# Kernel tuning notes

Measured on AMD Instinct MI355X. Metric: run time of the kernel, lower is better.

## Reference

```python
import jax, jax.numpy as jnp
import numpy as np

N, D = 4096, 784

def _conv_relu(x, w, b):
    y = jax.lax.conv_general_dilated(x, w, window_strides=(1, 1), padding='SAME',
                                     dimension_numbers=('NHWC', 'HWIO', 'NHWC'))
    return jax.nn.relu(y + b)

def _maxpool2(x):
    return jax.lax.reduce_window(x, -jnp.inf, jax.lax.max,
                                 (1, 2, 2, 1), (1, 2, 2, 1), 'SAME')

def _encoder(x, cw1, cb1, cw2, cb2, cw3, cb3, dw, db):
    h = x.reshape(-1, 28, 28, 1)
    h = _maxpool2(_conv_relu(h, cw1, cb1))   # [N,14,14,32]
    h = _maxpool2(_conv_relu(h, cw2, cb2))   # [N,7,7,32]
    h = _conv_relu(h, cw3, cb3)              # [N,7,7,16]
    h = h.reshape(h.shape[0], -1)            # [N,784]
    return h @ dw + db                       # [N,16]

def _pairwise_dist(a):
    # Euclidean cdist via Gram trick; avoids the O(N^2 * D) broadcasted diff.
    sq = jnp.sum(a * a, axis=-1)
    d2 = sq[:, None] + sq[None, :] - 2.0 * (a @ a.T)
    return jnp.sqrt(jnp.maximum(d2, 1e-12))

def setup_inputs() -> dict:
    key = jax.random.key(0)
    ks = jax.random.split(key, 5)
    return {
        'x':   jax.random.uniform(ks[0], (N, D), dtype=jnp.float32),
        'cw1': jax.random.normal(ks[1], (3, 3, 1, 32), dtype=jnp.float32) * 0.1,
        'cb1': jnp.zeros((32,), jnp.float32),
        'cw2': jax.random.normal(ks[2], (3, 3, 32, 32), dtype=jnp.float32) * 0.05,
        'cb2': jnp.zeros((32,), jnp.float32),
        'cw3': jax.random.normal(ks[3], (3, 3, 32, 16), dtype=jnp.float32) * 0.05,
        'cb3': jnp.zeros((16,), jnp.float32),
        'dw':  jax.random.normal(ks[4], (D, 16), dtype=jnp.float32) * 0.05,
        'db':  jnp.zeros((16,), jnp.float32),
        'nnfactor': 64,
    }

def reference(x, cw1, cb1, cw2, cb2, cw3, cb3, dw, db, nnfactor):
    n = x.shape[0]
    k = n // nnfactor  # as in train_step
    encoded = _encoder(x, cw1, cb1, cw2, cb2, cw3, cb3, dw, db)
    # tensor_get_nearest (faithful: tf.nn.top_k takes LARGEST distances)
    d_ini = _pairwise_dist(x)                       # [N,N]
    vals_ini, idx = jax.lax.top_k(d_ini, k - 1)     # sorted descending
    vals_ini = vals_ini[:, 1:]                      # [N,k-2]
    idx = idx[:, 1:]
    d_enc = _pairwise_dist(encoded)                 # [N,N]
    vals_enc = jnp.take_along_axis(d_enc, idx, axis=1)
    multiple = jnp.mean(vals_ini / vals_enc)
    reduced = vals_enc * multiple
    # per-row custom loss: max squared error, then mean over batch
    losses = jnp.max(jnp.square(vals_ini - reduced), axis=1)  # [N]
    total_loss = jnp.sum(losses) / n
    return total_loss
```

## Files before the change

kernel.cpp:

```cpp
#include <hip/hip_runtime.h>
#include <math.h>

#define NN 4096
#define DIM 784
#define K62 62
#define CAP 128

__global__ __launch_bounds__(256) void k_sqnorm(const float* __restrict__ x, double* __restrict__ sqnd,
                                                float* __restrict__ sqnf) {
    int r = blockIdx.x * 4 + (threadIdx.x >> 6);
    int lane = threadIdx.x & 63;
    const float* xr = x + (size_t)r * DIM;
    double s = 0.0;
    for (int k = lane; k < DIM; k += 64) { double v = (double)xr[k]; s += v * v; }
    for (int o = 32; o > 0; o >>= 1) s += __shfl_down(s, o);
    if (lane == 0) { sqnd[r] = s; sqnf[r] = (float)s; }
}

#define F4C(v, i) ((i) == 0 ? (v).x : (i) == 1 ? (v).y : (i) == 2 ? (v).z : (v).w)

__device__ __forceinline__ unsigned pk16(float a, float b) {
    return (__float_as_uint(a) >> 16) | (__float_as_uint(b) & 0xFFFF0000u);
}

__global__ __launch_bounds__(256, 4) void k_encgram(const float* __restrict__ x,
    const float* __restrict__ cw1, const float* __restrict__ cb1,
    const float* __restrict__ cw2, const float* __restrict__ cb2,
    const float* __restrict__ cw3, const float* __restrict__ cb3,
    const float* __restrict__ dw, const float* __restrict__ db,
    const float* __restrict__ sqnf,
    unsigned short* __restrict__ Dm16, double* __restrict__ Enc, double* __restrict__ esqd)
{
    __shared__ __align__(16) unsigned char SB[17408];
    int t = threadIdx.x;

    if (blockIdx.x < 1056) {
        float* As = (float*)SB;
        float* Bs = (float*)(SB + 8192);
        unsigned short* Cs16 = (unsigned short*)SB;
        int id = blockIdx.x >> 1, pass = blockIdx.x & 1;
        int bi = (int)((sqrtf(8.f * (float)id + 1.f) - 1.f) * 0.5f);
        while ((bi + 1) * (bi + 2) / 2 <= id) ++bi;
        while (bi * (bi + 1) / 2 > id) --bi;
        int bj = id - bi * (bi + 1) / 2;
        int i0 = bi * 128, j0 = bj * 128;
        int tx = t & 15, ty = t >> 4;
        int lrow = t >> 1, lk = (t & 1) * 8;
        int wl = lrow + ((lrow >> 5) << 2);
        int bofs = tx * 8 + ((tx >> 2) << 2);
        const float* arow = x + (size_t)(i0 + lrow) * DIM + lk;
        const float* brow = x + (size_t)(j0 + lrow) * DIM + lk;

        float acc[4][8];
        #pragma unroll
        for (int r = 0; r < 4; ++r)
        #pragma unroll
        for (int c = 0; c < 8; ++c) acc[r][c] = 0.f;
        int abase = ty * 8 + pass * 4;
        for (int kk = 0; kk < DIM; kk += 16) {
            float4 a0 = *(const float4*)(arow + kk);
            float4 a1 = *(const float4*)(arow + kk + 4);
            float4 b0 = *(const float4*)(brow + kk);
            float4 b1 = *(const float4*)(brow + kk + 4);
            __syncthreads();
            As[(lk + 0) * 128 + lrow] = a0.x; As[(lk + 1) * 128 + lrow] = a0.y;
            As[(lk + 2) * 128 + lrow] = a0.z; As[(lk + 3) * 128 + lrow] = a0.w;
            As[(lk + 4) * 128 + lrow] = a1.x; As[(lk + 5) * 128 + lrow] = a1.y;
            As[(lk + 6) * 128 + lrow] = a1.z; As[(lk + 7) * 128 + lrow] = a1.w;
            Bs[(lk + 0) * 140 + wl] = b0.x; Bs[(lk + 1) * 140 + wl] = b0.y;
            Bs[(lk + 2) * 140 + wl] = b0.z; Bs[(lk + 3) * 140 + wl] = b0.w;
            Bs[(lk + 4) * 140 + wl] = b1.x; Bs[(lk + 5) * 140 + wl] = b1.y;
            Bs[(lk + 6) * 140 + wl] = b1.z; Bs[(lk + 7) * 140 + wl] = b1.w;
            __syncthreads();
            #pragma unroll
            for (int k = 0; k < 16; ++k) {
                float4 av  = *(const float4*)&As[k * 128 + abase];
                const float* bp = &Bs[k * 140 + bofs];
                float4 bv0 = *(const float4*)bp;
                float4 bv1 = *(const float4*)(bp + 4);
                float a[4]  = {av.x, av.y, av.z, av.w};
                float bb[8] = {bv0.x, bv0.y, bv0.z, bv0.w, bv1.x, bv1.y, bv1.z, bv1.w};
                #pragma unroll
                for (int r = 0; r < 4; ++r)
                #pragma unroll
                for (int c = 0; c < 8; ++c) acc[r][c] = fmaf(a[r], bb[c], acc[r][c]);
            }
        }
        float si[4], sj[8];
        #pragma unroll
        for (int r = 0; r < 4; ++r) si[r] = sqnf[i0 + abase + r];
        #pragma unroll
        for (int c = 0; c < 8; ++c) sj[c] = sqnf[j0 + tx * 8 + c];
        #pragma unroll
        for (int r = 0; r < 4; ++r) {
            #pragma unroll
            for (int c = 0; c < 8; ++c) acc[r][c] = fmaxf(si[r] + sj[c] - 2.f * acc[r][c], 1e-12f);
            uint4 u;
            u.x = pk16(acc[r][0], acc[r][1]);
            u.y = pk16(acc[r][2], acc[r][3]);
            u.z = pk16(acc[r][4], acc[r][5]);
            u.w = pk16(acc[r][6], acc[r][7]);
            *(uint4*)(Dm16 + (size_t)(i0 + abase + r) * NN + j0 + tx * 8) = u;
        }
        if (bi != bj) {
            for (int qr = 0; qr < 2; ++qr)
            for (int qc = 0; qc < 2; ++qc) {
                __syncthreads();
                {
                    int a32 = t >> 3, c8 = t & 7;
                    int l = ((a32 >> 2) << 3) + pass * 4 + (a32 & 3);
                    uint4 v = *(const uint4*)&Dm16[(size_t)(i0 + qr * 64 + l) * NN + j0 + qc * 64 + c8 * 8];
                    int cb = c8 * 8;
                    Cs16[(cb + 0) * 36 + a32] = (unsigned short)(v.x);
                    Cs16[(cb + 1) * 36 + a32] = (unsigned short)(v.x >> 16);
                    Cs16[(cb + 2) * 36 + a32] = (unsigned short)(v.y);
                    Cs16[(cb + 3) * 36 + a32] = (unsigned short)(v.y >> 16);
                    Cs16[(cb + 4) * 36 + a32] = (unsigned short)(v.z);
                    Cs16[(cb + 5) * 36 + a32] = (unsigned short)(v.z >> 16);
                    Cs16[(cb + 6) * 36 + a32] = (unsigned short)(v.w);
                    Cs16[(cb + 7) * 36 + a32] = (unsigned short)(v.w >> 16);
                }
                __syncthreads();
                #pragma unroll
                for (int g = 0; g < 2; ++g) {
                    int idx = t + g * 256;
                    int a = idx >> 3, grp = idx & 7;
                    uint2 v = *(const uint2*)&Cs16[a * 36 + grp * 4];
                    *(uint2*)&Dm16[(size_t)(j0 + qc * 64 + a) * NN + i0 + qr * 64 + grp * 8 + pass * 4] = v;
                }
            }
        }
        return;
    }

    float*  sb1  = (float*)(SB);
    float*  sb2  = (float*)(SB + 128);
    float*  sb3  = (float*)(SB + 256);
    float*  sdb  = (float*)(SB + 320);
    float*  scw1 = (float*)(SB + 384);
    float*  wq   = (float*)(SB + 1536);
    float*  simg = (float*)(SB + 6144);
    float*  h1q  = (float*)(SB + 9744);
    float*  wq3  = (float*)(SB + 1536);
    float*  h2s  = (float*)(SB + 6144);
    float*  c3   = (float*)(SB + 6144);
    double* red  = (double*)(SB + 14768);
    double* se   = (double*)(SB + 16816);

    int n = blockIdx.x - 1056;
    for (int idx = t; idx < 1280; idx += 256) h1q[idx] = 0.f;
    for (int idx = t; idx < 900; idx += 256) simg[idx] = 0.f;
    __syncthreads();
    if (t < 196) {
        int row = t / 7, c4 = t % 7;
        float4 v = ((const float4*)(x + (size_t)n * DIM))[t];
        float* d = &simg[(row + 1) * 30 + 1 + c4 * 4];
        d[0] = v.x; d[1] = v.y; d[2] = v.z; d[3] = v.w;
    }
    for (int idx = t; idx < 288; idx += 256) scw1[idx] = cw1[idx];
    if (t < 32) { sb1[t] = cb1[t]; sb2[t] = cb2[t]; }
    if (t < 16) { sb3[t] = cb3[t]; sdb[t] = db[t]; }
    __syncthreads();

    int p2 = t >> 2, co8 = (t & 3) * 8;
    int py2 = p2 / 7, px2 = p2 % 7;
    int cbase = ((2 * py2) * 16 + 2 * px2) * 5;
    int ch1 = t & 3;
    float acc[4][8];
    if (t < 196) {
        #pragma unroll
        for (int pp = 0; pp < 4; ++pp)
        #pragma unroll
        for (int q = 0; q < 8; ++q) acc[pp][q] = sb2[co8 + q];
    }

    for (int oct = 0; oct < 8; ++oct) {
        __syncthreads();
        {
            int co = (oct << 2) + ch1;
            float wv[9];
            #pragma unroll
            for (int tp = 0; tp < 9; ++tp) wv[tp] = scw1[tp * 32 + co];
            float bias = sb1[co];
            for (int o = t; o < 784; o += 256) {
                int p = o >> 2;
                int py = p / 14, px = p % 14;
                float m = 0.f;
                #pragma unroll
                for (int dy = 0; dy < 2; ++dy)
                #pragma unroll
                for (int dx = 0; dx < 2; ++dx) {
                    const float* sp = &simg[(2 * py + dy + 1) * 30 + (2 * px + dx + 1)];
                    float a = bias;
                    a = fmaf(sp[-31], wv[0], a);
                    a = fmaf(sp[-30], wv[1], a);
                    a = fmaf(sp[-29], wv[2], a);
                    a = fmaf(sp[ -1], wv[3], a);
                    a = fmaf(sp[  0], wv[4], a);
                    a = fmaf(sp[  1], wv[5], a);
                    a = fmaf(sp[ 29], wv[6], a);
                    a = fmaf(sp[ 30], wv[7], a);
                    a = fmaf(sp[ 31], wv[8], a);
                    if (a < 0.f) a = 0.f;
                    if (a > m) m = a;
                }
                h1q[((py + 1) * 16 + (px + 1)) * 5 + ch1] = m;
            }
        }
        for (int w2 = t; w2 < 1152; w2 += 256) {
            int tap = w2 >> 7, k = w2 & 127;
            wq[w2] = cw2[tap * 1024 + oct * 128 + k];
        }
        __syncthreads();
        if (t < 196) {
            #pragma unroll
            for (int ky = 0; ky < 3; ++ky)
            #pragma unroll
            for (int kx = 0; kx < 3; ++kx) {
                const float* wb0 = &wq[(ky * 3 + kx) * 128 + co8];
                const float* hb = &h1q[cbase + (ky * 16 + kx) * 5];
                #pragma unroll
                for (int ci = 0; ci < 4; ++ci) {
                    float4 wA = *(const float4*)(wb0 + ci * 32);
                    float4 wB = *(const float4*)(wb0 + ci * 32 + 4);
                    float v00 = hb[ci];
                    float v01 = hb[5 + ci];
                    float v10 = hb[80 + ci];
                    float v11 = hb[85 + ci];
                    acc[0][0] = fmaf(v00, wA.x, acc[0][0]); acc[0][1] = fmaf(v00, wA.y, acc[0][1]);
                    acc[0][2] = fmaf(v00, wA.z, acc[0][2]); acc[0][3] = fmaf(v00, wA.w, acc[0][3]);
                    acc[0][4] = fmaf(v00, wB.x, acc[0][4]); acc[0][5] = fmaf(v00, wB.y, acc[0][5]);
                    acc[0][6] = fmaf(v00, wB.z, acc[0][6]); acc[0][7] = fmaf(v00, wB.w, acc[0][7]);
                    acc[1][0] = fmaf(v01, wA.x, acc[1][0]); acc[1][1] = fmaf(v01, wA.y, acc[1][1]);
                    acc[1][2] = fmaf(v01, wA.z, acc[1][2]); acc[1][3] = fmaf(v01, wA.w, acc[1][3]);
                    acc[1][4] = fmaf(v01, wB.x, acc[1][4]); acc[1][5] = fmaf(v01, wB.y, acc[1][5]);
                    acc[1][6] = fmaf(v01, wB.z, acc[1][6]); acc[1][7] = fmaf(v01, wB.w, acc[1][7]);
                    acc[2][0] = fmaf(v10, wA.x, acc[2][0]); acc[2][1] = fmaf(v10, wA.y, acc[2][1]);
                    acc[2][2] = fmaf(v10, wA.z, acc[2][2]); acc[2][3] = fmaf(v10, wA.w, acc[2][3]);
                    acc[2][4] = fmaf(v10, wB.x, acc[2][4]); acc[2][5] = fmaf(v10, wB.y, acc[2][5]);
                    acc[2][6] = fmaf(v10, wB.z, acc[2][6]); acc[2][7] = fmaf(v10, wB.w, acc[2][7]);
                    acc[3][0] = fmaf(v11, wA.x, acc[3][0]); acc[3][1] = fmaf(v11, wA.y, acc[3][1]);
                    acc[3][2] = fmaf(v11, wA.z, acc[3][2]); acc[3][3] = fmaf(v11, wA.w, acc[3][3]);
                    acc[3][4] = fmaf(v11, wB.x, acc[3][4]); acc[3][5] = fmaf(v11, wB.y, acc[3][5]);
                    acc[3][6] = fmaf(v11, wB.z, acc[3][6]); acc[3][7] = fmaf(v11, wB.w, acc[3][7]);
                }
            }
        }
    }
    __syncthreads();
    if (t < 196) {
        float mm[8];
        #pragma unroll
        for (int q = 0; q < 8; ++q) {
            float m = 0.f;
            #pragma unroll
            for (int pp = 0; pp < 4; ++pp) {
                float a = acc[pp][q];
                if (a < 0.f) a = 0.f;
                if (a > m) m = a;
            }
            mm[q] = m;
        }
        *(float4*)&h2s[p2 * 44 + co8]     = make_float4(mm[0], mm[1], mm[2], mm[3]);
        *(float4*)&h2s[p2 * 44 + co8 + 4] = make_float4(mm[4], mm[5], mm[6], mm[7]);
    }
    float a0 = 0.f, a1 = 0.f, a2 = 0.f, a3 = 0.f;
    int p3 = t >> 2, co4 = (t & 3) * 4;
    int py3 = p3 / 7, px3 = p3 % 7;
    if (t < 196) {
        a0 = sb3[co4]; a1 = sb3[co4 + 1];
        a2 = sb3[co4 + 2]; a3 = sb3[co4 + 3];
    }
    for (int qq = 0; qq < 4; ++qq) {
        __syncthreads();
        for (int w2 = t; w2 < 1152; w2 += 256) {
            int tap = w2 >> 7, k = w2 & 127;
            wq3[w2] = cw3[tap * 512 + qq * 128 + k];
        }
        __syncthreads();
        if (t < 196) {
            for (int ky = 0; ky < 3; ++ky) {
                int iy = py3 + ky - 1; if ((unsigned)iy >= 7u) continue;
                for (int kx = 0; kx < 3; ++kx) {
                    int ix = px3 + kx - 1; if ((unsigned)ix >= 7u) continue;
                    const float* hp = &h2s[(iy * 7 + ix) * 44 + qq * 8];
                    float4 h0 = *(const float4*)hp;
                    float4 h1 = *(const float4*)(hp + 4);
                    const float* wp = &wq3[(ky * 3 + kx) * 128 + co4];
                    #pragma unroll
                    for (int ci = 0; ci < 8; ++ci) {
                        float av = (ci < 4) ? F4C(h0, ci) : F4C(h1, ci - 4);
                        float4 wv = *(const float4*)(wp + ci * 16);
                        a0 = fmaf(av, wv.x, a0); a1 = fmaf(av, wv.y, a1);
                        a2 = fmaf(av, wv.z, a2); a3 = fmaf(av, wv.w, a3);
                    }
                }
            }
        }
    }
    __syncthreads();
    if (t < 196) {
        float r0 = a0 > 0.f ? a0 : 0.f, r1 = a1 > 0.f ? a1 : 0.f;
        float r2 = a2 > 0.f ? a2 : 0.f, r3 = a3 > 0.f ? a3 : 0.f;
        *(float4*)&c3[p3 * 16 + co4] = make_float4(r0, r1, r2, r3);
    }
    __syncthreads();
    {
        int part = t >> 4, o = t & 15, j0 = part * 49;
        double s = 0.0;
        for (int j = 0; j < 49; ++j) s = fma((double)c3[j0 + j], (double)dw[(size_t)(j0 + j) * 16 + o], s);
        red[part * 16 + o] = s;
    }
    __syncthreads();
    if (t < 16) {
        double e = (double)sdb[t];
        for (int q = 0; q < 16; ++q) e += red[q * 16 + t];
        Enc[(size_t)n * 16 + t] = e;
        se[t] = e;
    }
    __syncthreads();
    if (t == 0) {
        double s = 0.0;
        for (int q = 0; q < 16; ++q) s += se[q] * se[q];
        esqd[n] = s;
    }
}

__global__ __launch_bounds__(256) void k_topsel(const unsigned short* __restrict__ Dm16,
                                                const double* __restrict__ sqnd,
                                                const float* __restrict__ x,
                                                double* __restrict__ topvd, int* __restrict__ topi) {
    __shared__ float xi[DIM];
    __shared__ unsigned wsum[8];
    __shared__ int cj[CAP];
    __shared__ double cvd[CAP];
    __shared__ unsigned ncnt;
    int i = blockIdx.x, t = threadIdx.x;
    const unsigned* drow = (const unsigned*)(Dm16 + (size_t)i * NN);
    unsigned uk[8];
    #pragma unroll
    for (int s = 0; s < 8; ++s) {
        int wd = t + s * 256;
        unsigned u = drow[wd];
        if (2 * wd == i)     u &= 0xFFFF0000u;
        if (2 * wd + 1 == i) u &= 0x0000FFFFu;
        uk[s] = u;
    }
    if (t < 196) ((float4*)xi)[t] = ((const float4*)(x + (size_t)i * DIM))[t];
    if (t == 0) ncnt = 0;
    int lane = t & 63, w = t >> 6;
    unsigned lo = 0u, hi = 0xFFFFu;
    for (int it = 0; it < 16; ++it) {
        unsigned mid = (lo + hi + 1u) >> 1;
        unsigned cnt = 0;
        #pragma unroll
        for (int s = 0; s < 8; ++s) {
            cnt += ((uk[s] & 0xFFFFu) >= mid) ? 1u : 0u;
            cnt += ((uk[s] >> 16) >= mid) ? 1u : 0u;
        }
        #pragma unroll
        for (int off = 32; off > 0; off >>= 1) cnt += __shfl_down(cnt, off);
        if (lane == 0) wsum[(it & 1) * 4 + w] = cnt;
        __syncthreads();
        int bb = (it & 1) * 4;
        unsigned tot = wsum[bb] + wsum[bb + 1] + wsum[bb + 2] + wsum[bb + 3];
        if (tot >= 63u) lo = mid; else hi = mid - 1u;
    }
    unsigned prefix = lo;
    #pragma unroll
    for (int s = 0; s < 8; ++s) {
        int wd = t + s * 256;
        if ((uk[s] & 0xFFFFu) >= prefix) {
            unsigned p = atomicAdd(&ncnt, 1u);
            if (p < CAP) cj[p] = 2 * wd;
        }
        if ((uk[s] >> 16) >= prefix) {
            unsigned p = atomicAdd(&ncnt, 1u);
            if (p < CAP) cj[p] = 2 * wd + 1;
        }
    }
    __syncthreads();
    int ncand = min((int)ncnt, CAP);
    double sqi_d = sqnd[i];
    const float4* xi4 = (const float4*)xi;
    int g = t >> 4, gl = t & 15;
    for (int c = g; c < ncand; c += 16) {
        const float4* xj4 = (const float4*)(x + (size_t)cj[c] * DIM);
        double s = 0.0;
        for (int k = gl; k < 196; k += 16) {
            float4 a = xi4[k]; float4 b = xj4[k];
            s = fma((double)a.x, (double)b.x, s);
            s = fma((double)a.y, (double)b.y, s);
            s = fma((double)a.z, (double)b.z, s);
            s = fma((double)a.w, (double)b.w, s);
        }
        #pragma unroll
        for (int o = 8; o > 0; o >>= 1) s += __shfl_down(s, o, 16);
        if (gl == 0) cvd[c] = sqrt(fmax(sqi_d + sqnd[cj[c]] - 2.0 * s, 1e-12));
    }
    __syncthreads();
    if (t < ncand) {
        double v = cvd[t]; int jj = cj[t];
        int r = 0;
        for (int c2 = 0; c2 < ncand; ++c2) {
            double v2 = cvd[c2];
            if (v2 > v || (v2 == v && cj[c2] < jj)) ++r;
        }
        if (r >= 1 && r < 63) {
            topvd[(size_t)i * K62 + r - 1] = v;
            topi[(size_t)i * K62 + r - 1] = jj;
        }
    }
}

__global__ __launch_bounds__(256) void k_ratio(const double* __restrict__ Enc, const double* __restrict__ esqd,
                                               const double* __restrict__ topvd, const int* __restrict__ topi,
                                               double* __restrict__ vencd, double* __restrict__ Sp) {
    __shared__ double wp[4];
    int r = blockIdx.x * 4 + (threadIdx.x >> 6);
    int lane = threadIdx.x & 63, w = threadIdx.x >> 6;
    double ratio = 0.0;
    if (lane < K62) {
        int j = topi[(size_t)r * K62 + lane];
        const double* Er = Enc + (size_t)r * 16;
        const double* Ej = Enc + (size_t)j * 16;
        double dot = 0.0;
        #pragma unroll
        for (int q = 0; q < 16; ++q) dot = fma(Er[q], Ej[q], dot);
        double ve = sqrt(fmax(esqd[r] + esqd[j] - 2.0 * dot, 1e-12));
        vencd[(size_t)r * K62 + lane] = ve;
        ratio = topvd[(size_t)r * K62 + lane] / ve;
    }
    for (int o = 32; o > 0; o >>= 1) ratio += __shfl_down(ratio, o);
    if (lane == 0) wp[w] = ratio;
    __syncthreads();
    if (threadIdx.x == 0) Sp[blockIdx.x] = wp[0] + wp[1] + wp[2] + wp[3];
}

__global__ __launch_bounds__(256) void k_loss(const double* __restrict__ topvd, const double* __restrict__ vencd,
                                              const double* __restrict__ Sp, double* __restrict__ Lp) {
    __shared__ double wp[4];
    __shared__ double wq2[4];
    int t = threadIdx.x;
    int lane = t & 63, w = t >> 6;
    double sp = Sp[t] + Sp[t + 256] + Sp[t + 512] + Sp[t + 768];
    for (int o = 32; o > 0; o >>= 1) sp += __shfl_down(sp, o);
    if (lane == 0) wp[w] = sp;
    __syncthreads();
    double m = (wp[0] + wp[1] + wp[2] + wp[3]) * (1.0 / (4096.0 * 62.0));
    int r = blockIdx.x * 4 + w;
    double v = -1.0;
    if (lane < K62) {
        double d = topvd[(size_t)r * K62 + lane] - m * vencd[(size_t)r * K62 + lane];
        v = d * d;
    }
    for (int o = 32; o > 0; o >>= 1) { double ov = __shfl_down(v, o); v = (ov > v) ? ov : v; }
    if (lane == 0) wq2[w] = v;
    __syncthreads();
    if (t == 0) Lp[blockIdx.x] = wq2[0] + wq2[1] + wq2[2] + wq2[3];
}

__global__ __launch_bounds__(256) void k_final(const double* __restrict__ Lp, float* __restrict__ out) {
    __shared__ double wp[4];
    int t = threadIdx.x, lane = t & 63, w = t >> 6;
    double s = Lp[t] + Lp[t + 256] + Lp[t + 512] + Lp[t + 768];
    for (int o = 32; o > 0; o >>= 1) s += __shfl_down(s, o);
    if (lane == 0) wp[w] = s;
    __syncthreads();
    if (t == 0) out[0] = (float)((wp[0] + wp[1] + wp[2] + wp[3]) * (1.0 / 4096.0));
}

extern "C" void kernel_launch(void* const* d_in, const int* in_sizes, int n_in,
                              void* d_out, int out_size, void* d_ws, size_t ws_size,
                              hipStream_t stream) {
    const float* x   = (const float*)d_in[0];
    const float* cw1 = (const float*)d_in[1];
    const float* cb1 = (const float*)d_in[2];
    const float* cw2 = (const float*)d_in[3];
    const float* cb2 = (const float*)d_in[4];
    const float* cw3 = (const float*)d_in[5];
    const float* cb3 = (const float*)d_in[6];
    const float* dw  = (const float*)d_in[7];
    const float* db  = (const float*)d_in[8];

    char* wsb = (char*)d_ws;
    unsigned short* Dm16 = (unsigned short*)wsb;
    double* Enc   = (double*)(wsb + 33554432);
    double* esqd  = (double*)(wsb + 34078720);
    double* sqnd  = (double*)(wsb + 34111488);
    float*  sqnf  = (float*)(wsb + 34144256);
    double* topvd = (double*)(wsb + 34160640);
    double* vencd = (double*)(wsb + 36192256);
    int*    topi  = (int*)(wsb + 38223872);
    double* Sp    = (double*)(wsb + 39239680);
    double* Lp    = (double*)(wsb + 39247872);
    float*  out   = (float*)d_out;

    k_sqnorm<<<1024, 256, 0, stream>>>(x, sqnd, sqnf);
    k_encgram<<<5152, 256, 0, stream>>>(x, cw1, cb1, cw2, cb2, cw3, cb3, dw, db,
                                        sqnf, Dm16, Enc, esqd);
    k_topsel<<<4096, 256, 0, stream>>>(Dm16, sqnd, x, topvd, topi);
    k_ratio<<<1024, 256, 0, stream>>>(Enc, esqd, topvd, topi, vencd, Sp);
    k_loss<<<1024, 256, 0, stream>>>(topvd, vencd, Sp, Lp);
    k_final<<<1, 256, 0, stream>>>(Lp, out);
}
```

Baseline: 666.5 us.

## Split fused encoder/gram kernel; compute full 128x128 Gram tile per 512-thread block

The combined encoder+Gram kernel is split into two kernels. The Gram kernel now uses 512-thread blocks that each compute a full 128x128 tile, where before two 256-thread blocks each computed half the rows. This halves redundant loads of the B tile and makes the transpose write-back use full 16-byte stores. The cost is that encoder blocks and Gram blocks no longer run concurrently in one launch, and only 528 Gram blocks are launched, which may underfill the GPU.

```diff
diff --git a/kernel.cpp b/kernel.cpp
--- a/kernel.cpp
+++ b/kernel.cpp
@@ -23,116 +23,106 @@
     return (__float_as_uint(a) >> 16) | (__float_as_uint(b) & 0xFFFF0000u);
 }
 
-__global__ __launch_bounds__(256, 4) void k_encgram(const float* __restrict__ x,
+__global__ __launch_bounds__(512, 4) void k_gram(const float* __restrict__ x,
+                                                 const float* __restrict__ sqnf,
+                                                 unsigned short* __restrict__ Dm16) {
+    __shared__ __align__(16) unsigned char SB[17408];
+    float* As = (float*)SB;
+    float* Bs = (float*)(SB + 8192);
+    unsigned short* Cs16 = (unsigned short*)SB;
+    int t = threadIdx.x;
+    int id = blockIdx.x;
+    int bi = (int)((sqrtf(8.f * (float)id + 1.f) - 1.f) * 0.5f);
+    while ((bi + 1) * (bi + 2) / 2 <= id) ++bi;
+    while (bi * (bi + 1) / 2 > id) --bi;
+    int bj = id - bi * (bi + 1) / 2;
+    int i0 = bi * 128, j0 = bj * 128;
+    int tx = t & 15, ty = t >> 4;
+    int lrow = t >> 2, lk = (t & 3) * 4;
+    int wl = lrow + ((lrow >> 5) << 2);
+    int bofs = tx * 8 + ((tx >> 2) << 2);
+    const float* arow = x + (size_t)(i0 + lrow) * DIM + lk;
+    const float* brow = x + (size_t)(j0 + lrow) * DIM + lk;
+
+    float acc[4][8];
+    #pragma unroll
+    for (int r = 0; r < 4; ++r)
+    #pragma unroll
+    for (int c = 0; c < 8; ++c) acc[r][c] = 0.f;
+
+    for (int kk = 0; kk < DIM; kk += 16) {
+        float4 a0 = *(const float4*)(arow + kk);
+        float4 b0 = *(const float4*)(brow + kk);
+        __syncthreads();
+        As[(lk + 0) * 128 + lrow] = a0.x; As[(lk + 1) * 128 + lrow] = a0.y;
+        As[(lk + 2) * 128 + lrow] = a0.z; As[(lk + 3) * 128 + lrow] = a0.w;
+        Bs[(lk + 0) * 140 + wl] = b0.x; Bs[(lk + 1) * 140 + wl] = b0.y;
+        Bs[(lk + 2) * 140 + wl] = b0.z; Bs[(lk + 3) * 140 + wl] = b0.w;
+        __syncthreads();
+        #pragma unroll
+        for (int k = 0; k < 16; ++k) {
+            float4 av  = *(const float4*)&As[k * 128 + ty * 4];
+            const float* bp = &Bs[k * 140 + bofs];
+            float4 bv0 = *(const float4*)bp;
+            float4 bv1 = *(const float4*)(bp + 4);
+            float a[4]  = {av.x, av.y, av.z, av.w};
+            float bb[8] = {bv0.x, bv0.y, bv0.z, bv0.w, bv1.x, bv1.y, bv1.z, bv1.w};
+            #pragma unroll
+            for (int r = 0; r < 4; ++r)
+            #pragma unroll
+            for (int c = 0; c < 8; ++c) acc[r][c] = fmaf(a[r], bb[c], acc[r][c]);
+        }
+    }
+    float si[4], sj[8];
+    #pragma unroll
+    for (int r = 0; r < 4; ++r) si[r] = sqnf[i0 + ty * 4 + r];
+    #pragma unroll
+    for (int c = 0; c < 8; ++c) sj[c] = sqnf[j0 + tx * 8 + c];
+    #pragma unroll
+    for (int r = 0; r < 4; ++r) {
+        #pragma unroll
+        for (int c = 0; c < 8; ++c) acc[r][c] = fmaxf(si[r] + sj[c] - 2.f * acc[r][c], 1e-12f);
+        uint4 u;
+        u.x = pk16(acc[r][0], acc[r][1]);
+        u.y = pk16(acc[r][2], acc[r][3]);
+        u.z = pk16(acc[r][4], acc[r][5]);
+        u.w = pk16(acc[r][6], acc[r][7]);
+        *(uint4*)(Dm16 + (size_t)(i0 + ty * 4 + r) * NN + j0 + tx * 8) = u;
+    }
+    if (bi != bj) {
+        for (int qr = 0; qr < 2; ++qr)
+        for (int qc = 0; qc < 2; ++qc) {
+            __syncthreads();
+            {
+                int a = t >> 3, c8 = t & 7;
+                uint4 v = *(const uint4*)&Dm16[(size_t)(i0 + qr * 64 + a) * NN + j0 + qc * 64 + c8 * 8];
+                Cs16[(c8 * 8 + 0) * 72 + a] = (unsigned short)(v.x);
+                Cs16[(c8 * 8 + 1) * 72 + a] = (unsigned short)(v.x >> 16);
+                Cs16[(c8 * 8 + 2) * 72 + a] = (unsigned short)(v.y);
+                Cs16[(c8 * 8 + 3) * 72 + a] = (unsigned short)(v.y >> 16);
+                Cs16[(c8 * 8 + 4) * 72 + a] = (unsigned short)(v.z);
+                Cs16[(c8 * 8 + 5) * 72 + a] = (unsigned short)(v.z >> 16);
+                Cs16[(c8 * 8 + 6) * 72 + a] = (unsigned short)(v.w);
+                Cs16[(c8 * 8 + 7) * 72 + a] = (unsigned short)(v.w >> 16);
+            }
+            __syncthreads();
+            {
+                int a = t >> 3, c8 = t & 7;
+                uint4 v = *(const uint4*)&Cs16[a * 72 + c8 * 8];
+                *(uint4*)&Dm16[(size_t)(j0 + qc * 64 + a) * NN + i0 + qr * 64 + c8 * 8] = v;
+            }
+        }
+    }
+}
+
+__global__ __launch_bounds__(256, 4) void k_encoder(const float* __restrict__ x,
     const float* __restrict__ cw1, const float* __restrict__ cb1,
     const float* __restrict__ cw2, const float* __restrict__ cb2,
     const float* __restrict__ cw3, const float* __restrict__ cb3,
     const float* __restrict__ dw, const float* __restrict__ db,
-    const float* __restrict__ sqnf,
-    unsigned short* __restrict__ Dm16, double* __restrict__ Enc, double* __restrict__ esqd)
+    double* __restrict__ Enc, double* __restrict__ esqd)
 {
     __shared__ __align__(16) unsigned char SB[17408];
-    int t = threadIdx.x;
-
-    if (blockIdx.x < 1056) {
-        float* As = (float*)SB;
-        float* Bs = (float*)(SB + 8192);
-        unsigned short* Cs16 = (unsigned short*)SB;
-        int id = blockIdx.x >> 1, pass = blockIdx.x & 1;
-        int bi = (int)((sqrtf(8.f * (float)id + 1.f) - 1.f) * 0.5f);
-        while ((bi + 1) * (bi + 2) / 2 <= id) ++bi;
-        while (bi * (bi + 1) / 2 > id) --bi;
-        int bj = id - bi * (bi + 1) / 2;
-        int i0 = bi * 128, j0 = bj * 128;
-        int tx = t & 15, ty = t >> 4;
-        int lrow = t >> 1, lk = (t & 1) * 8;
-        int wl = lrow + ((lrow >> 5) << 2);
-        int bofs = tx * 8 + ((tx >> 2) << 2);
-        const float* arow = x + (size_t)(i0 + lrow) * DIM + lk;
-        const float* brow = x + (size_t)(j0 + lrow) * DIM + lk;
-
-        float acc[4][8];
-        #pragma unroll
-        for (int r = 0; r < 4; ++r)
-        #pragma unroll
-        for (int c = 0; c < 8; ++c) acc[r][c] = 0.f;
-        int abase = ty * 8 + pass * 4;
-        for (int kk = 0; kk < DIM; kk += 16) {
-            float4 a0 = *(const float4*)(arow + kk);
-            float4 a1 = *(const float4*)(arow + kk + 4);
-            float4 b0 = *(const float4*)(brow + kk);
-            float4 b1 = *(const float4*)(brow + kk + 4);
-            __syncthreads();
-            As[(lk + 0) * 128 + lrow] = a0.x; As[(lk + 1) * 128 + lrow] = a0.y;
-            As[(lk + 2) * 128 + lrow] = a0.z; As[(lk + 3) * 128 + lrow] = a0.w;
-            As[(lk + 4) * 128 + lrow] = a1.x; As[(lk + 5) * 128 + lrow] = a1.y;
-            As[(lk + 6) * 128 + lrow] = a1.z; As[(lk + 7) * 128 + lrow] = a1.w;
-            Bs[(lk + 0) * 140 + wl] = b0.x; Bs[(lk + 1) * 140 + wl] = b0.y;
-            Bs[(lk + 2) * 140 + wl] = b0.z; Bs[(lk + 3) * 140 + wl] = b0.w;
-            Bs[(lk + 4) * 140 + wl] = b1.x; Bs[(lk + 5) * 140 + wl] = b1.y;
-            Bs[(lk + 6) * 140 + wl] = b1.z; Bs[(lk + 7) * 140 + wl] = b1.w;
-            __syncthreads();
-            #pragma unroll
-            for (int k = 0; k < 16; ++k) {
-                float4 av  = *(const float4*)&As[k * 128 + abase];
-                const float* bp = &Bs[k * 140 + bofs];
-                float4 bv0 = *(const float4*)bp;
-                float4 bv1 = *(const float4*)(bp + 4);
-                float a[4]  = {av.x, av.y, av.z, av.w};
-                float bb[8] = {bv0.x, bv0.y, bv0.z, bv0.w, bv1.x, bv1.y, bv1.z, bv1.w};
-                #pragma unroll
-                for (int r = 0; r < 4; ++r)
-                #pragma unroll
-                for (int c = 0; c < 8; ++c) acc[r][c] = fmaf(a[r], bb[c], acc[r][c]);
-            }
-        }
-        float si[4], sj[8];
-        #pragma unroll
-        for (int r = 0; r < 4; ++r) si[r] = sqnf[i0 + abase + r];
-        #pragma unroll
-        for (int c = 0; c < 8; ++c) sj[c] = sqnf[j0 + tx * 8 + c];
-        #pragma unroll
-        for (int r = 0; r < 4; ++r) {
-            #pragma unroll
-            for (int c = 0; c < 8; ++c) acc[r][c] = fmaxf(si[r] + sj[c] - 2.f * acc[r][c], 1e-12f);
-            uint4 u;
-            u.x = pk16(acc[r][0], acc[r][1]);
-            u.y = pk16(acc[r][2], acc[r][3]);
-            u.z = pk16(acc[r][4], acc[r][5]);
-            u.w = pk16(acc[r][6], acc[r][7]);
-            *(uint4*)(Dm16 + (size_t)(i0 + abase + r) * NN + j0 + tx * 8) = u;
-        }
-        if (bi != bj) {
-            for (int qr = 0; qr < 2; ++qr)
-            for (int qc = 0; qc < 2; ++qc) {
-                __syncthreads();
-                {
-                    int a32 = t >> 3, c8 = t & 7;
-                    int l = ((a32 >> 2) << 3) + pass * 4 + (a32 & 3);
-                    uint4 v = *(const uint4*)&Dm16[(size_t)(i0 + qr * 64 + l) * NN + j0 + qc * 64 + c8 * 8];
-                    int cb = c8 * 8;
-                    Cs16[(cb + 0) * 36 + a32] = (unsigned short)(v.x);
-                    Cs16[(cb + 1) * 36 + a32] = (unsigned short)(v.x >> 16);
-                    Cs16[(cb + 2) * 36 + a32] = (unsigned short)(v.y);
-                    Cs16[(cb + 3) * 36 + a32] = (unsigned short)(v.y >> 16);
-                    Cs16[(cb + 4) * 36 + a32] = (unsigned short)(v.z);
-                    Cs16[(cb + 5) * 36 + a32] = (unsigned short)(v.z >> 16);
-                    Cs16[(cb + 6) * 36 + a32] = (unsigned short)(v.w);
-                    Cs16[(cb + 7) * 36 + a32] = (unsigned short)(v.w >> 16);
-                }
-                __syncthreads();
-                #pragma unroll
-                for (int g = 0; g < 2; ++g) {
-                    int idx = t + g * 256;
-                    int a = idx >> 3, grp = idx & 7;
-                    uint2 v = *(const uint2*)&Cs16[a * 36 + grp * 4];
-                    *(uint2*)&Dm16[(size_t)(j0 + qc * 64 + a) * NN + i0 + qr * 64 + grp * 8 + pass * 4] = v;
-                }
-            }
-        }
-        return;
-    }
-
     float*  sb1  = (float*)(SB);
     float*  sb2  = (float*)(SB + 128);
     float*  sb3  = (float*)(SB + 256);
@@ -147,7 +137,8 @@
     double* red  = (double*)(SB + 14768);
     double* se   = (double*)(SB + 16816);
 
-    int n = blockIdx.x - 1056;
+    int t = threadIdx.x;
+    int n = blockIdx.x;
     for (int idx = t; idx < 1280; idx += 256) h1q[idx] = 0.f;
     for (int idx = t; idx < 900; idx += 256) simg[idx] = 0.f;
     __syncthreads();
@@ -497,8 +488,8 @@
     float*  out   = (float*)d_out;
 
     k_sqnorm<<<1024, 256, 0, stream>>>(x, sqnd, sqnf);
-    k_encgram<<<5152, 256, 0, stream>>>(x, cw1, cb1, cw2, cb2, cw3, cb3, dw, db,
-                                        sqnf, Dm16, Enc, esqd);
+    k_gram<<<528, 512, 0, stream>>>(x, sqnf, Dm16);
+    k_encoder<<<4096, 256, 0, stream>>>(x, cw1, cb1, cw2, cb2, cw3, cb3, dw, db, Enc, esqd);
     k_topsel<<<4096, 256, 0, stream>>>(Dm16, sqnd, x, topvd, topi);
     k_ratio<<<1024, 256, 0, stream>>>(Enc, esqd, topvd, topi, vencd, Sp);
     k_loss<<<1024, 256, 0, stream>>>(topvd, vencd, Sp, Lp);
```

Measured after the change: 727.5 us. 1.09x slower.

## Merge two half-row gram passes into one block per tile with wider transpose

Applied to the files above, without the earlier changes.

Each 128x128 Gram tile was split across two blocks, one per half of the row subset. Now a single block loops over both passes and computes the full tile, then transposes the whole 64x64 quadrant with 16-byte shared-memory reads and global writes instead of 8-byte half-strided ones. This halves the number of gram blocks and widens the mirrored stores. The cost is that each block does twice the serial work, which lowers the available parallelism. The A and B tiles are also loaded from global memory twice inside one block.

```diff
diff --git a/kernel.cpp b/kernel.cpp
--- a/kernel.cpp
+++ b/kernel.cpp
@@ -34,11 +34,11 @@
     __shared__ __align__(16) unsigned char SB[17408];
     int t = threadIdx.x;
 
-    if (blockIdx.x < 1056) {
+    if (blockIdx.x < 528) {
         float* As = (float*)SB;
         float* Bs = (float*)(SB + 8192);
         unsigned short* Cs16 = (unsigned short*)SB;
-        int id = blockIdx.x >> 1, pass = blockIdx.x & 1;
+        int id = blockIdx.x;
         int bi = (int)((sqrtf(8.f * (float)id + 1.f) - 1.f) * 0.5f);
         while ((bi + 1) * (bi + 2) / 2 <= id) ++bi;
         while (bi * (bi + 1) / 2 > id) --bi;
@@ -51,82 +51,84 @@
         const float* arow = x + (size_t)(i0 + lrow) * DIM + lk;
         const float* brow = x + (size_t)(j0 + lrow) * DIM + lk;
 
-        float acc[4][8];
-        #pragma unroll
-        for (int r = 0; r < 4; ++r)
-        #pragma unroll
-        for (int c = 0; c < 8; ++c) acc[r][c] = 0.f;
-        int abase = ty * 8 + pass * 4;
-        for (int kk = 0; kk < DIM; kk += 16) {
-            float4 a0 = *(const float4*)(arow + kk);
-            float4 a1 = *(const float4*)(arow + kk + 4);
-            float4 b0 = *(const float4*)(brow + kk);
-            float4 b1 = *(const float4*)(brow + kk + 4);
-            __syncthreads();
-            As[(lk + 0) * 128 + lrow] = a0.x; As[(lk + 1) * 128 + lrow] = a0.y;
-            As[(lk + 2) * 128 + lrow] = a0.z; As[(lk + 3) * 128 + lrow] = a0.w;
-            As[(lk + 4) * 128 + lrow] = a1.x; As[(lk + 5) * 128 + lrow] = a1.y;
-            As[(lk + 6) * 128 + lrow] = a1.z; As[(lk + 7) * 128 + lrow] = a1.w;
-            Bs[(lk + 0) * 140 + wl] = b0.x; Bs[(lk + 1) * 140 + wl] = b0.y;
-            Bs[(lk + 2) * 140 + wl] = b0.z; Bs[(lk + 3) * 140 + wl] = b0.w;
-            Bs[(lk + 4) * 140 + wl] = b1.x; Bs[(lk + 5) * 140 + wl] = b1.y;
-            Bs[(lk + 6) * 140 + wl] = b1.z; Bs[(lk + 7) * 140 + wl] = b1.w;
-            __syncthreads();
-            #pragma unroll
-            for (int k = 0; k < 16; ++k) {
-                float4 av  = *(const float4*)&As[k * 128 + abase];
-                const float* bp = &Bs[k * 140 + bofs];
-                float4 bv0 = *(const float4*)bp;
-                float4 bv1 = *(const float4*)(bp + 4);
-                float a[4]  = {av.x, av.y, av.z, av.w};
-                float bb[8] = {bv0.x, bv0.y, bv0.z, bv0.w, bv1.x, bv1.y, bv1.z, bv1.w};
-                #pragma unroll
-                for (int r = 0; r < 4; ++r)
-                #pragma unroll
-                for (int c = 0; c < 8; ++c) acc[r][c] = fmaf(a[r], bb[c], acc[r][c]);
-            }
-        }
-        float si[4], sj[8];
-        #pragma unroll
-        for (int r = 0; r < 4; ++r) si[r] = sqnf[i0 + abase + r];
-        #pragma unroll
-        for (int c = 0; c < 8; ++c) sj[c] = sqnf[j0 + tx * 8 + c];
-        #pragma unroll
-        for (int r = 0; r < 4; ++r) {
-            #pragma unroll
-            for (int c = 0; c < 8; ++c) acc[r][c] = fmaxf(si[r] + sj[c] - 2.f * acc[r][c], 1e-12f);
-            uint4 u;
-            u.x = pk16(acc[r][0], acc[r][1]);
-            u.y = pk16(acc[r][2], acc[r][3]);
-            u.z = pk16(acc[r][4], acc[r][5]);
-            u.w = pk16(acc[r][6], acc[r][7]);
-            *(uint4*)(Dm16 + (size_t)(i0 + abase + r) * NN + j0 + tx * 8) = u;
+        for (int pass = 0; pass < 2; ++pass) {
+            float acc[4][8];
+            #pragma unroll
+            for (int r = 0; r < 4; ++r)
+            #pragma unroll
+            for (int c = 0; c < 8; ++c) acc[r][c] = 0.f;
+            int abase = ty * 8 + pass * 4;
+            for (int kk = 0; kk < DIM; kk += 16) {
+                float4 a0 = *(const float4*)(arow + kk);
+                float4 a1 = *(const float4*)(arow + kk + 4);
+                float4 b0 = *(const float4*)(brow + kk);
+                float4 b1 = *(const float4*)(brow + kk + 4);
+                __syncthreads();
+                As[(lk + 0) * 128 + lrow] = a0.x; As[(lk + 1) * 128 + lrow] = a0.y;
+                As[(lk + 2) * 128 + lrow] = a0.z; As[(lk + 3) * 128 + lrow] = a0.w;
+                As[(lk + 4) * 128 + lrow] = a1.x; As[(lk + 5) * 128 + lrow] = a1.y;
+                As[(lk + 6) * 128 + lrow] = a1.z; As[(lk + 7) * 128 + lrow] = a1.w;
+                Bs[(lk + 0) * 140 + wl] = b0.x; Bs[(lk + 1) * 140 + wl] = b0.y;
+                Bs[(lk + 2) * 140 + wl] = b0.z; Bs[(lk + 3) * 140 + wl] = b0.w;
+                Bs[(lk + 4) * 140 + wl] = b1.x; Bs[(lk + 5) * 140 + wl] = b1.y;
+                Bs[(lk + 6) * 140 + wl] = b1.z; Bs[(lk + 7) * 140 + wl] = b1.w;
+                __syncthreads();
+                #pragma unroll
+                for (int k = 0; k < 16; ++k) {
+                    float4 av  = *(const float4*)&As[k * 128 + abase];
+                    const float* bp = &Bs[k * 140 + bofs];
+                    float4 bv0 = *(const float4*)bp;
+                    float4 bv1 = *(const float4*)(bp + 4);
+                    float a[4]  = {av.x, av.y, av.z, av.w};
+                    float bb[8] = {bv0.x, bv0.y, bv0.z, bv0.w, bv1.x, bv1.y, bv1.z, bv1.w};
+                    #pragma unroll
+                    for (int r = 0; r < 4; ++r)
+                    #pragma unroll
+                    for (int c = 0; c < 8; ++c) acc[r][c] = fmaf(a[r], bb[c], acc[r][c]);
+                }
+            }
+            float si[4], sj[8];
+            #pragma unroll
+            for (int r = 0; r < 4; ++r) si[r] = sqnf[i0 + abase + r];
+            #pragma unroll
+            for (int c = 0; c < 8; ++c) sj[c] = sqnf[j0 + tx * 8 + c];
+            #pragma unroll
+            for (int r = 0; r < 4; ++r) {
+                #pragma unroll
+                for (int c = 0; c < 8; ++c) acc[r][c] = fmaxf(si[r] + sj[c] - 2.f * acc[r][c], 1e-12f);
+                uint4 u;
+                u.x = pk16(acc[r][0], acc[r][1]);
+                u.y = pk16(acc[r][2], acc[r][3]);
+                u.z = pk16(acc[r][4], acc[r][5]);
+                u.w = pk16(acc[r][6], acc[r][7]);
+                *(uint4*)(Dm16 + (size_t)(i0 + abase + r) * NN + j0 + tx * 8) = u;
+            }
         }
         if (bi != bj) {
             for (int qr = 0; qr < 2; ++qr)
             for (int qc = 0; qc < 2; ++qc) {
                 __syncthreads();
-                {
-                    int a32 = t >> 3, c8 = t & 7;
-                    int l = ((a32 >> 2) << 3) + pass * 4 + (a32 & 3);
-                    uint4 v = *(const uint4*)&Dm16[(size_t)(i0 + qr * 64 + l) * NN + j0 + qc * 64 + c8 * 8];
-                    int cb = c8 * 8;
-                    Cs16[(cb + 0) * 36 + a32] = (unsigned short)(v.x);
-                    Cs16[(cb + 1) * 36 + a32] = (unsigned short)(v.x >> 16);
-                    Cs16[(cb + 2) * 36 + a32] = (unsigned short)(v.y);
-                    Cs16[(cb + 3) * 36 + a32] = (unsigned short)(v.y >> 16);
-                    Cs16[(cb + 4) * 36 + a32] = (unsigned short)(v.z);
-                    Cs16[(cb + 5) * 36 + a32] = (unsigned short)(v.z >> 16);
-                    Cs16[(cb + 6) * 36 + a32] = (unsigned short)(v.w);
-                    Cs16[(cb + 7) * 36 + a32] = (unsigned short)(v.w >> 16);
+                #pragma unroll
+                for (int g = 0; g < 2; ++g) {
+                    int idx = t + g * 256;
+                    int a = idx >> 3, c8 = idx & 7;
+                    uint4 v = *(const uint4*)&Dm16[(size_t)(i0 + qr * 64 + a) * NN + j0 + qc * 64 + c8 * 8];
+                    Cs16[(c8 * 8 + 0) * 72 + a] = (unsigned short)(v.x);
+                    Cs16[(c8 * 8 + 1) * 72 + a] = (unsigned short)(v.x >> 16);
+                    Cs16[(c8 * 8 + 2) * 72 + a] = (unsigned short)(v.y);
+                    Cs16[(c8 * 8 + 3) * 72 + a] = (unsigned short)(v.y >> 16);
+                    Cs16[(c8 * 8 + 4) * 72 + a] = (unsigned short)(v.z);
+                    Cs16[(c8 * 8 + 5) * 72 + a] = (unsigned short)(v.z >> 16);
+                    Cs16[(c8 * 8 + 6) * 72 + a] = (unsigned short)(v.w);
+                    Cs16[(c8 * 8 + 7) * 72 + a] = (unsigned short)(v.w >> 16);
                 }
                 __syncthreads();
                 #pragma unroll
                 for (int g = 0; g < 2; ++g) {
                     int idx = t + g * 256;
-                    int a = idx >> 3, grp = idx & 7;
-                    uint2 v = *(const uint2*)&Cs16[a * 36 + grp * 4];
-                    *(uint2*)&Dm16[(size_t)(j0 + qc * 64 + a) * NN + i0 + qr * 64 + grp * 8 + pass * 4] = v;
+                    int a = idx >> 3, c8 = idx & 7;
+                    uint4 v = *(const uint4*)&Cs16[a * 72 + c8 * 8];
+                    *(uint4*)&Dm16[(size_t)(j0 + qc * 64 + a) * NN + i0 + qr * 64 + c8 * 8] = v;
                 }
             }
         }
@@ -147,7 +149,7 @@
     double* red  = (double*)(SB + 14768);
     double* se   = (double*)(SB + 16816);
 
-    int n = blockIdx.x - 1056;
+    int n = blockIdx.x - 528;
     for (int idx = t; idx < 1280; idx += 256) h1q[idx] = 0.f;
     for (int idx = t; idx < 900; idx += 256) simg[idx] = 0.f;
     __syncthreads();
@@ -497,7 +499,7 @@
     float*  out   = (float*)d_out;
 
     k_sqnorm<<<1024, 256, 0, stream>>>(x, sqnd, sqnf);
-    k_encgram<<<5152, 256, 0, stream>>>(x, cw1, cb1, cw2, cb2, cw3, cb3, dw, db,
+    k_encgram<<<4624, 256, 0, stream>>>(x, cw1, cb1, cw2, cb2, cw3, cb3, dw, db,
                                         sqnf, Dm16, Enc, esqd);
     k_topsel<<<4096, 256, 0, stream>>>(Dm16, sqnd, x, topvd, topi);
     k_ratio<<<1024, 256, 0, stream>>>(Enc, esqd, topvd, topi, vencd, Sp);
```

New measurement: 663.6 us. Within noise of the previous version (-0.4%).
